# Kernel optimization log

Hardware: AMD Instinct MI355X
Metric: run time of the kernel (lower is better)

The kernel has to match this reference:

```python
import jax, jax.numpy as jnp
import numpy as np

N = 50000      # areaNum
E = 64         # embeddingsize
NE = 800000    # nonzeros of normalized adjacency
WK = 9         # walk_length + 1
L = 2          # args.L
TMP = 0.5      # args.choosing_tmp
BIAS = 1e-4


def _logistic_noise(k, shape):
    # eps ~ U(bias, 1-bias); noise = log(eps) - log(1-eps)
    u = jax.random.uniform(k, shape, minval=BIAS, maxval=1.0 - BIAS)
    return jnp.log(u) - jnp.log1p(-u)


def setup_inputs() -> dict:
    key = jax.random.key(0)
    ks = jax.random.split(key, 16)
    rng = np.random.default_rng(0)

    # ---- normalized sparse adjacency (D^-1/2 A D^-1/2), COO sorted by row ----
    row = np.sort(rng.integers(0, N, NE))
    col = rng.integers(0, N, NE)
    deg = np.bincount(row, minlength=N).astype(np.float32)
    dinv = np.where(deg > 0, deg ** -0.5, 0.0).astype(np.float32)
    vals = dinv[row] * dinv[col]

    # ---- random-walk mean-pooling adjacency, row-normalized ----
    rw_row = np.repeat(np.arange(N), WK)
    rw_col = rng.integers(0, N, N * WK)
    rw_col[::WK] = np.arange(N)  # walk starts at self
    rw_vals = np.full(N * WK, 1.0 / WK, dtype=np.float32)

    def lin(k, fan_in, shape):
        return jax.random.normal(k, shape, dtype=jnp.float32) / np.sqrt(fan_in)

    inp = {
        'x': jax.random.normal(ks[0], (N, E), dtype=jnp.float32),
        'vals': jnp.asarray(vals),
        'rw_vals': jnp.asarray(rw_vals),
        't_W1': lin(ks[1], 2 * E, (L, 2 * E, E)),
        't_b1': jnp.zeros((L, E), jnp.float32),
        't_W2': lin(ks[2], E, (L, E, 1)),
        't_b2': jnp.zeros((L, 1), jnp.float32),
        's_W1': lin(ks[3], E, (L, E, E)),
        's_b1': jnp.zeros((L, E), jnp.float32),
        's_W2': lin(ks[4], E, (L, E, 1)),
        's_b2': jnp.zeros((L, 1), jnp.float32),
        't_noise': _logistic_noise(ks[5], (L, NE)),
        's_noise': _logistic_noise(ks[6], (L, N, 1)),
        'row': jnp.asarray(row, dtype=jnp.int64) if jax.config.jax_enable_x64 else jnp.asarray(row, dtype=jnp.int32),
        'col': jnp.asarray(col, dtype=jnp.int32),
        'rw_row': jnp.asarray(rw_row, dtype=jnp.int32),
        'rw_col': jnp.asarray(rw_col, dtype=jnp.int32),
    }
    inp['row'] = jnp.asarray(row, dtype=jnp.int32)
    return inp


def reference(x, vals, rw_vals, t_W1, t_b1, t_W2, t_b2, s_W1, s_b1, s_W2, s_b2,
              t_noise, s_noise, row, col, rw_row, rw_col):
    n = x.shape[0]

    def spmm(r, c, v, h):  # sparse [n,n] @ dense [n,E]
        return jax.ops.segment_sum(v[:, None] * h[c], r, num_segments=n)

    # per-edge concat of ORIGINAL embeddings (same tensor every layer, as in source)
    t_cat = jnp.concatenate([x[row], x[col]], axis=-1)  # [nE, 2E]

    # --- mask-learning pass ---
    cur = x
    t_masks, s_masks = [], []
    for i in range(L):
        cur = spmm(row, col, vals, cur)
        t_h = jax.nn.relu(t_cat @ t_W1[i] + t_b1[i])
        t_logit = t_h @ t_W2[i] + t_b2[i]                      # [nE,1]
        t_m = jax.nn.sigmoid((t_noise[i][:, None] + t_logit) / TMP)[:, 0]
        t_masks.append(t_m)
        s_h = jax.nn.relu(cur @ s_W1[i] + s_b1[i])
        s_logit = s_h @ s_W2[i] + s_b2[i]                      # [N,1]
        s_masks.append(jax.nn.sigmoid((s_noise[i] + s_logit) / TMP))

    # --- t branch: gated spmm propagation, mean over layers ---
    cur_t = x
    acc_t = x
    for i in range(L):
        cur_t = spmm(row, col, vals * t_masks[i], cur_t)
        acc_t = acc_t + cur_t
    emb_t = acc_t / (L + 1)

    # --- s branch: gated mix with random-walk mean pooling, then spmm ---
    cur_s = x
    acc_s = x
    s_reg = jnp.float32(0.0)
    for i in range(L):
        mp = spmm(rw_row, rw_col, rw_vals, cur_s)
        cur_s = s_masks[i] * cur_s + (1.0 - s_masks[i]) * mp
        cur_s = spmm(row, col, vals, cur_s)
        acc_s = acc_s + cur_s
        s_reg = s_reg + s_masks[i].sum() / n
    emb_s = acc_s / (L + 1)
    s_reg = s_reg / L
    t_reg = jnp.float32(0.0)  # source never accumulates into t_reg
    return emb_t, emb_s, t_reg, s_reg, t_masks[-1]
```

## Files before the change

### kernel.cpp

```cpp
#include <hip/hip_runtime.h>

#define NNODES 50000
#define EDIM 64
#define WKLEN 9
#define NEDGE 800000
#define NPAD (NNODES + 64)

using bf16x8 = __attribute__((ext_vector_type(8))) __bf16;
using f32x4  = __attribute__((ext_vector_type(4))) float;

__device__ __align__(256) unsigned short g_xbf[NPAD * EDIM];
__device__ __align__(256) unsigned short g_ABh[NNODES * 128];
__device__ __align__(256) unsigned short g_c1h[NPAD * EDIM];
__device__ __align__(256) unsigned short g_c2h[NPAD * EDIM];
__device__ __align__(256) unsigned short g_g0h[NNODES * EDIM];
__device__ __align__(256) unsigned short g_sc1h[NNODES * EDIM];
__device__ __align__(256) unsigned short g_Pr[NNODES * 128];
__device__ __align__(256) unsigned short g_Pc[NNODES * 128];
__device__ __align__(256) float g_mt0[NEDGE];
__device__ __align__(256) float g_mt1[NEDGE];
__device__ __align__(256) float g_sm0[NNODES];
__device__ __align__(256) float g_sm1[NNODES];
__device__ __align__(256) int   g_rowptr[NNODES + 1];
__device__ __align__(256) unsigned short g_Tswz[2048 * 8];
__device__ __align__(256) unsigned short g_Sswz[1024 * 8];

__device__ __forceinline__ unsigned short f2bf(float f) {
    union { float f; unsigned int i; } v;
    v.f = f;
    unsigned int r = v.i + 0x7FFFu + ((v.i >> 16) & 1u);
    return (unsigned short)(r >> 16);
}
__device__ __forceinline__ float bf2f_lo(unsigned int u) {
    union { unsigned int i; float f; } v; v.i = u << 16; return v.f;
}
__device__ __forceinline__ float bf2f_hi(unsigned int u) {
    union { unsigned int i; float f; } v; v.i = u & 0xFFFF0000u; return v.f;
}

__global__ __launch_bounds__(256) void misc_kernel(
    const float* __restrict__ x, const float* __restrict__ tW1,
    const float* __restrict__ sW1, const int* __restrict__ row,
    int n, int nE)
{
    int bid = blockIdx.x, tid = threadIdx.x;
    if (bid < 1563) {
        int i = bid * 256 + tid;
        if (i < NNODES * EDIM / 8) {
            const float* src = x + i * 8;
            union { unsigned short s[8]; uint4 q; } u;
#pragma unroll
            for (int j = 0; j < 8; ++j) u.s[j] = f2bf(src[j]);
            *(uint4*)&g_xbf[i * 8] = u.q;
        }
    } else if (bid < 1759) {
        int i = (bid - 1563) * 256 + tid;
        if (i > n) return;
        int lo = 0, hi = nE;
        while (lo < hi) {
            int mid = (lo + hi) >> 1;
            if (row[mid] < i) lo = mid + 1; else hi = mid;
        }
        g_rowptr[i] = lo;
    } else if (bid < 1767) {
        int t = (bid - 1759) * 256 + tid;
        int s = t >> 9, f = (t >> 6) & 7, ln = t & 63;
        int li = s >> 1, half = s & 1, ks = f >> 2, nn = f & 3;
        int q = ln >> 4, mcl = ln & 15;
        union { unsigned short sv[8]; uint4 q4; } u;
#pragma unroll
        for (int j = 0; j < 8; ++j) {
            int kg = half * 64 + ks * 32 + q * 8 + j;
            u.sv[j] = f2bf(tW1[li * 8192 + kg * 64 + nn * 16 + mcl]);
        }
        *(uint4*)&g_Tswz[t * 8] = u.q4;
    } else {
        int t = (bid - 1767) * 256 + tid;
        int li = t >> 9, ks = (t >> 8) & 1, nn = (t >> 6) & 3, ln = t & 63;
        int q = ln >> 4, mcl = ln & 15;
        union { unsigned short sv[8]; uint4 q4; } u;
#pragma unroll
        for (int j = 0; j < 8; ++j)
            u.sv[j] = f2bf(sW1[li * 4096 + (ks * 32 + q * 8 + j) * 64 + nn * 16 + mcl]);
        *(uint4*)&g_Sswz[t * 8] = u.q4;
    }
}

__global__ __launch_bounds__(256) void prep2_kernel(int n)
{
    int tid = threadIdx.x;
    int wave = tid >> 6, lane = tid & 63;
    int mc = lane & 15, quad = lane >> 4;
    int nb = blockIdx.x * 64 + wave * 16;
    const unsigned short* bp = g_xbf + (nb + mc) * 64 + quad * 8;
    bf16x8 af0 = *(const bf16x8*)bp;
    bf16x8 af1 = *(const bf16x8*)(bp + 32);
    const f32x4 zero = {0.f, 0.f, 0.f, 0.f};
#pragma unroll
    for (int s = 0; s < 4; ++s) {
        int li = s >> 1, half = s & 1;
        f32x4 acc[4];
#pragma unroll
        for (int nn = 0; nn < 4; ++nn) acc[nn] = zero;
#pragma unroll
        for (int nn = 0; nn < 4; ++nn) {
            bf16x8 b0 = *(const bf16x8*)&g_Tswz[((s * 8 + nn) * 64 + lane) * 8];
            bf16x8 b1 = *(const bf16x8*)&g_Tswz[((s * 8 + 4 + nn) * 64 + lane) * 8];
            acc[nn] = __builtin_amdgcn_mfma_f32_16x16x32_bf16(af0, b0, acc[nn], 0, 0, 0);
            acc[nn] = __builtin_amdgcn_mfma_f32_16x16x32_bf16(af1, b1, acc[nn], 0, 0, 0);
        }
        unsigned short* dst = half ? g_Pc : g_Pr;
#pragma unroll
        for (int nn = 0; nn < 4; ++nn)
#pragma unroll
            for (int r = 0; r < 4; ++r) {
                int node = nb + quad * 4 + r;
                if (node < n)
                    dst[node * 128 + li * 64 + nn * 16 + mc] = f2bf(acc[nn][r]);
            }
    }
}

__global__ __launch_bounds__(256) void edge_mask_kernel(
    const float* __restrict__ tb1, const float* __restrict__ tW2,
    const float* __restrict__ tb2, const float* __restrict__ tnoise,
    const int* __restrict__ row, const int* __restrict__ col,
    float* __restrict__ mask_out, int nE)
{
    int tid = threadIdx.x;
    int lane = tid & 63;
    int sub = lane & 7;
    int eg = lane >> 3;
    int wv = (blockIdx.x * 256 + tid) >> 6;
    int e = wv * 8 + eg;

    float b1_0[8], b1_1[8], w2_0[8], w2_1[8];
    *(float4*)&b1_0[0] = *(const float4*)&tb1[sub * 8];
    *(float4*)&b1_0[4] = *(const float4*)&tb1[sub * 8 + 4];
    *(float4*)&b1_1[0] = *(const float4*)&tb1[64 + sub * 8];
    *(float4*)&b1_1[4] = *(const float4*)&tb1[64 + sub * 8 + 4];
    *(float4*)&w2_0[0] = *(const float4*)&tW2[sub * 8];
    *(float4*)&w2_0[4] = *(const float4*)&tW2[sub * 8 + 4];
    *(float4*)&w2_1[0] = *(const float4*)&tW2[64 + sub * 8];
    *(float4*)&w2_1[4] = *(const float4*)&tW2[64 + sub * 8 + 4];

    int rn = row[e], cn = col[e];
    uint4 qr0 = *(const uint4*)&g_Pr[rn * 128 + sub * 8];
    uint4 qr1 = *(const uint4*)&g_Pr[rn * 128 + 64 + sub * 8];
    uint4 qc0 = *(const uint4*)&g_Pc[cn * 128 + sub * 8];
    uint4 qc1 = *(const uint4*)&g_Pc[cn * 128 + 64 + sub * 8];

    float p0 = 0.f, p1 = 0.f;
    unsigned r0[4] = {qr0.x, qr0.y, qr0.z, qr0.w};
    unsigned r1[4] = {qr1.x, qr1.y, qr1.z, qr1.w};
    unsigned c0[4] = {qc0.x, qc0.y, qc0.z, qc0.w};
    unsigned c1[4] = {qc1.x, qc1.y, qc1.z, qc1.w};
#pragma unroll
    for (int k = 0; k < 4; ++k) {
        float hA = fmaxf(bf2f_lo(r0[k]) + bf2f_lo(c0[k]) + b1_0[2 * k], 0.f);
        float hB = fmaxf(bf2f_hi(r0[k]) + bf2f_hi(c0[k]) + b1_0[2 * k + 1], 0.f);
        p0 = fmaf(hA, w2_0[2 * k], p0);
        p0 = fmaf(hB, w2_0[2 * k + 1], p0);
        float gA = fmaxf(bf2f_lo(r1[k]) + bf2f_lo(c1[k]) + b1_1[2 * k], 0.f);
        float gB = fmaxf(bf2f_hi(r1[k]) + bf2f_hi(c1[k]) + b1_1[2 * k + 1], 0.f);
        p1 = fmaf(gA, w2_1[2 * k], p1);
        p1 = fmaf(gB, w2_1[2 * k + 1], p1);
    }
#pragma unroll
    for (int off = 1; off <= 4; off <<= 1) {
        p0 += __shfl_xor(p0, off, 64);
        p1 += __shfl_xor(p1, off, 64);
    }
    if (sub == 0) {
        float z0 = (tnoise[e] + p0 + tb2[0]) * 2.0f;
        float m0 = 1.0f / (1.0f + expf(-z0));
        g_mt0[e] = m0;
        float z1 = (tnoise[nE + e] + p1 + tb2[1]) * 2.0f;
        float m1 = 1.0f / (1.0f + expf(-z1));
        g_mt1[e] = m1;
        mask_out[e] = m1;
    }
}

__device__ __forceinline__ void nm_body(
    int bid, const unsigned short* __restrict__ cur, int li,
    const float* __restrict__ b1, const float* __restrict__ W2,
    const float* __restrict__ b2, const float* __restrict__ noise,
    float* __restrict__ smout, int n)
{
    int tid = threadIdx.x;
    int wave = tid >> 6, lane = tid & 63;
    int mc = lane & 15, quad = lane >> 4;
    int nb = bid * 64 + wave * 16;
    const unsigned short* basep = cur + (nb + mc) * 64 + quad * 8;
    bf16x8 af0 = *(const bf16x8*)basep;
    bf16x8 af1 = *(const bf16x8*)(basep + 32);
    f32x4 acc[4];
    const f32x4 zero = {0.f, 0.f, 0.f, 0.f};
#pragma unroll
    for (int nn = 0; nn < 4; ++nn) acc[nn] = zero;
#pragma unroll
    for (int nn = 0; nn < 4; ++nn) {
        bf16x8 b0 = *(const bf16x8*)&g_Sswz[((li * 8 + nn) * 64 + lane) * 8];
        bf16x8 b1f = *(const bf16x8*)&g_Sswz[((li * 8 + 4 + nn) * 64 + lane) * 8];
        acc[nn] = __builtin_amdgcn_mfma_f32_16x16x32_bf16(af0, b0, acc[nn], 0, 0, 0);
        acc[nn] = __builtin_amdgcn_mfma_f32_16x16x32_bf16(af1, b1f, acc[nn], 0, 0, 0);
    }
    float p[4];
#pragma unroll
    for (int r = 0; r < 4; ++r) {
        float s = 0.f;
#pragma unroll
        for (int nn = 0; nn < 4; ++nn) {
            float h = acc[nn][r] + b1[nn * 16 + mc];
            s = fmaf(fmaxf(h, 0.f), W2[nn * 16 + mc], s);
        }
        p[r] = s;
    }
#pragma unroll
    for (int off = 8; off >= 1; off >>= 1)
#pragma unroll
        for (int r = 0; r < 4; ++r) p[r] += __shfl_xor(p[r], off, 64);
    if (mc == 0) {
        float b2v = b2[0];
#pragma unroll
        for (int r = 0; r < 4; ++r) {
            int node = nb + quad * 4 + r;
            if (node < n) {
                float z = (noise[node] + p[r] + b2v) * 2.0f;
                smout[node] = 1.0f / (1.0f + expf(-z));
            }
        }
    }
}

__global__ __launch_bounds__(256) void s1_kernel(
    const int* __restrict__ colv, const float* __restrict__ vals, int n)
{
    int w = blockIdx.x * 8 + (threadIdx.x >> 5);
    int d2 = threadIdx.x & 31;
    int s = g_rowptr[w], e = g_rowptr[w + 1];
    float pl[4] = {0.f, 0.f, 0.f, 0.f}, ph[4] = {0.f, 0.f, 0.f, 0.f};
    float ql[4] = {0.f, 0.f, 0.f, 0.f}, qh[4] = {0.f, 0.f, 0.f, 0.f};
    int j = s;
    for (; j + 3 < e; j += 4) {
        int c0 = colv[j], c1 = colv[j + 1], c2 = colv[j + 2], c3 = colv[j + 3];
        unsigned u0 = *(const unsigned*)&g_xbf[c0 * 64 + 2 * d2];
        unsigned u1 = *(const unsigned*)&g_xbf[c1 * 64 + 2 * d2];
        unsigned u2 = *(const unsigned*)&g_xbf[c2 * 64 + 2 * d2];
        unsigned u3 = *(const unsigned*)&g_xbf[c3 * 64 + 2 * d2];
        float v0 = vals[j], v1 = vals[j + 1], v2 = vals[j + 2], v3 = vals[j + 3];
        float m0 = g_mt0[j], m1 = g_mt0[j + 1], m2 = g_mt0[j + 2], m3 = g_mt0[j + 3];
        float vm0 = v0 * m0, vm1 = v1 * m1, vm2 = v2 * m2, vm3 = v3 * m3;
        pl[0] = fmaf(v0, bf2f_lo(u0), pl[0]); ph[0] = fmaf(v0, bf2f_hi(u0), ph[0]);
        ql[0] = fmaf(vm0, bf2f_lo(u0), ql[0]); qh[0] = fmaf(vm0, bf2f_hi(u0), qh[0]);
        pl[1] = fmaf(v1, bf2f_lo(u1), pl[1]); ph[1] = fmaf(v1, bf2f_hi(u1), ph[1]);
        ql[1] = fmaf(vm1, bf2f_lo(u1), ql[1]); qh[1] = fmaf(vm1, bf2f_hi(u1), qh[1]);
        pl[2] = fmaf(v2, bf2f_lo(u2), pl[2]); ph[2] = fmaf(v2, bf2f_hi(u2), ph[2]);
        ql[2] = fmaf(vm2, bf2f_lo(u2), ql[2]); qh[2] = fmaf(vm2, bf2f_hi(u2), qh[2]);
        pl[3] = fmaf(v3, bf2f_lo(u3), pl[3]); ph[3] = fmaf(v3, bf2f_hi(u3), ph[3]);
        ql[3] = fmaf(vm3, bf2f_lo(u3), ql[3]); qh[3] = fmaf(vm3, bf2f_hi(u3), qh[3]);
    }
    for (; j < e; ++j) {
        int c = colv[j]; float v = vals[j], m = g_mt0[j];
        unsigned u = *(const unsigned*)&g_xbf[c * 64 + 2 * d2];
        float vm = v * m;
        pl[0] = fmaf(v, bf2f_lo(u), pl[0]); ph[0] = fmaf(v, bf2f_hi(u), ph[0]);
        ql[0] = fmaf(vm, bf2f_lo(u), ql[0]); qh[0] = fmaf(vm, bf2f_hi(u), qh[0]);
    }
    float p0 = (pl[0] + pl[1]) + (pl[2] + pl[3]);
    float p1 = (ph[0] + ph[1]) + (ph[2] + ph[3]);
    float q0 = (ql[0] + ql[1]) + (ql[2] + ql[3]);
    float q1 = (qh[0] + qh[1]) + (qh[2] + qh[3]);
    uint2 pk;
    pk.x = (unsigned)f2bf(p0) | ((unsigned)f2bf(q0) << 16);
    pk.y = (unsigned)f2bf(p1) | ((unsigned)f2bf(q1) << 16);
    *(uint2*)&g_ABh[w * 128 + 4 * d2] = pk;
    *(unsigned*)&g_c1h[w * 64 + 2 * d2] =
        (unsigned)f2bf(p0) | ((unsigned)f2bf(p1) << 16);
}

__global__ __launch_bounds__(256) void s2_nm0_kernel(
    const int* __restrict__ colv, const float* __restrict__ vals,
    const float* __restrict__ x, float* __restrict__ emb_t,
    const float* __restrict__ sb1, const float* __restrict__ sW2,
    const float* __restrict__ sb2, const float* __restrict__ snz, int n)
{
    if (blockIdx.x >= 6250) {
        nm_body(blockIdx.x - 6250, g_c1h, 0, sb1, sW2, sb2, snz, g_sm0, n);
        return;
    }
    int w = blockIdx.x * 8 + (threadIdx.x >> 5);
    int d2 = threadIdx.x & 31;
    int s = g_rowptr[w], e = g_rowptr[w + 1];
    float cl[4] = {0.f, 0.f, 0.f, 0.f}, ch[4] = {0.f, 0.f, 0.f, 0.f};
    float tl[4] = {0.f, 0.f, 0.f, 0.f}, th[4] = {0.f, 0.f, 0.f, 0.f};
    int j = s;
    for (; j + 3 < e; j += 4) {
        int c0 = colv[j], c1 = colv[j + 1], c2 = colv[j + 2], c3 = colv[j + 3];
        uint2 U0 = *(const uint2*)&g_ABh[c0 * 128 + 4 * d2];
        uint2 U1 = *(const uint2*)&g_ABh[c1 * 128 + 4 * d2];
        uint2 U2 = *(const uint2*)&g_ABh[c2 * 128 + 4 * d2];
        uint2 U3 = *(const uint2*)&g_ABh[c3 * 128 + 4 * d2];
        float v0 = vals[j], v1 = vals[j + 1], v2 = vals[j + 2], v3 = vals[j + 3];
        float m0 = g_mt1[j], m1 = g_mt1[j + 1], m2 = g_mt1[j + 2], m3 = g_mt1[j + 3];
        float vm0 = v0 * m0, vm1 = v1 * m1, vm2 = v2 * m2, vm3 = v3 * m3;
        cl[0] = fmaf(v0, bf2f_lo(U0.x), cl[0]); tl[0] = fmaf(vm0, bf2f_hi(U0.x), tl[0]);
        ch[0] = fmaf(v0, bf2f_lo(U0.y), ch[0]); th[0] = fmaf(vm0, bf2f_hi(U0.y), th[0]);
        cl[1] = fmaf(v1, bf2f_lo(U1.x), cl[1]); tl[1] = fmaf(vm1, bf2f_hi(U1.x), tl[1]);
        ch[1] = fmaf(v1, bf2f_lo(U1.y), ch[1]); th[1] = fmaf(vm1, bf2f_hi(U1.y), th[1]);
        cl[2] = fmaf(v2, bf2f_lo(U2.x), cl[2]); tl[2] = fmaf(vm2, bf2f_hi(U2.x), tl[2]);
        ch[2] = fmaf(v2, bf2f_lo(U2.y), ch[2]); th[2] = fmaf(vm2, bf2f_hi(U2.y), th[2]);
        cl[3] = fmaf(v3, bf2f_lo(U3.x), cl[3]); tl[3] = fmaf(vm3, bf2f_hi(U3.x), tl[3]);
        ch[3] = fmaf(v3, bf2f_lo(U3.y), ch[3]); th[3] = fmaf(vm3, bf2f_hi(U3.y), th[3]);
    }
    for (; j < e; ++j) {
        int c = colv[j]; float v = vals[j], m = g_mt1[j];
        uint2 U = *(const uint2*)&g_ABh[c * 128 + 4 * d2];
        float vm = v * m;
        cl[0] = fmaf(v, bf2f_lo(U.x), cl[0]); tl[0] = fmaf(vm, bf2f_hi(U.x), tl[0]);
        ch[0] = fmaf(v, bf2f_lo(U.y), ch[0]); th[0] = fmaf(vm, bf2f_hi(U.y), th[0]);
    }
    float c0s = (cl[0] + cl[1]) + (cl[2] + cl[3]);
    float c1s = (ch[0] + ch[1]) + (ch[2] + ch[3]);
    float t0s = (tl[0] + tl[1]) + (tl[2] + tl[3]);
    float t1s = (th[0] + th[1]) + (th[2] + th[3]);
    int o2 = w * 64 + 2 * d2;
    uint2 U2v = *(const uint2*)&g_ABh[w * 128 + 4 * d2];
    float2 et;
    et.x = (x[o2]     + bf2f_hi(U2v.x) + t0s) * (1.0f / 3.0f);
    et.y = (x[o2 + 1] + bf2f_hi(U2v.y) + t1s) * (1.0f / 3.0f);
    *(float2*)&emb_t[o2] = et;
    *(unsigned*)&g_c2h[o2] = (unsigned)f2bf(c0s) | ((unsigned)f2bf(c1s) << 16);
}

__device__ __forceinline__ void rw_body(
    int bid, const int* __restrict__ rw_col, const float* __restrict__ rwv,
    const unsigned short* __restrict__ cur, const float* __restrict__ smask,
    unsigned short* __restrict__ outg)
{
    int w = bid * 8 + (threadIdx.x >> 5);
    int d2 = threadIdx.x & 31;
    int base = w * WKLEN;
    float a0 = 0.f, a1 = 0.f;
#pragma unroll
    for (int j = 0; j < WKLEN; ++j) {
        int c = rw_col[base + j];
        float v = rwv[base + j];
        unsigned u = *(const unsigned*)&cur[c * 64 + 2 * d2];
        a0 = fmaf(v, bf2f_lo(u), a0);
        a1 = fmaf(v, bf2f_hi(u), a1);
    }
    float sm = smask[w];
    unsigned u = *(const unsigned*)&cur[w * 64 + 2 * d2];
    float r0 = sm * bf2f_lo(u) + (1.f - sm) * a0;
    float r1 = sm * bf2f_hi(u) + (1.f - sm) * a1;
    *(unsigned*)&outg[w * 64 + 2 * d2] =
        (unsigned)f2bf(r0) | ((unsigned)f2bf(r1) << 16);
}

__global__ __launch_bounds__(256) void rw0_nm1_kernel(
    const int* __restrict__ rw_col, const float* __restrict__ rwv,
    const float* __restrict__ sb1, const float* __restrict__ sW2,
    const float* __restrict__ sb2, const float* __restrict__ snz, int n)
{
    if (blockIdx.x >= 6250) {
        nm_body(blockIdx.x - 6250, g_c2h, 1, sb1, sW2, sb2, snz, g_sm1, n);
        return;
    }
    rw_body(blockIdx.x, rw_col, rwv, g_xbf, g_sm0, g_g0h);
}

__device__ __forceinline__ void spmm_body(
    int bid, const int* __restrict__ colv, const float* __restrict__ vals,
    const unsigned short* __restrict__ h, float* __restrict__ l0,
    float* __restrict__ l1, int* __restrict__ wout, int* __restrict__ d2out)
{
    int w = bid * 8 + (threadIdx.x >> 5);
    int d2 = threadIdx.x & 31;
    int s = g_rowptr[w], e = g_rowptr[w + 1];
    float al[4] = {0.f, 0.f, 0.f, 0.f}, ah[4] = {0.f, 0.f, 0.f, 0.f};
    int j = s;
    for (; j + 3 < e; j += 4) {
        int c0 = colv[j], c1 = colv[j + 1], c2 = colv[j + 2], c3 = colv[j + 3];
        unsigned u0 = *(const unsigned*)&h[c0 * 64 + 2 * d2];
        unsigned u1 = *(const unsigned*)&h[c1 * 64 + 2 * d2];
        unsigned u2 = *(const unsigned*)&h[c2 * 64 + 2 * d2];
        unsigned u3 = *(const unsigned*)&h[c3 * 64 + 2 * d2];
        float v0 = vals[j], v1 = vals[j + 1], v2 = vals[j + 2], v3 = vals[j + 3];
        al[0] = fmaf(v0, bf2f_lo(u0), al[0]); ah[0] = fmaf(v0, bf2f_hi(u0), ah[0]);
        al[1] = fmaf(v1, bf2f_lo(u1), al[1]); ah[1] = fmaf(v1, bf2f_hi(u1), ah[1]);
        al[2] = fmaf(v2, bf2f_lo(u2), al[2]); ah[2] = fmaf(v2, bf2f_hi(u2), ah[2]);
        al[3] = fmaf(v3, bf2f_lo(u3), al[3]); ah[3] = fmaf(v3, bf2f_hi(u3), ah[3]);
    }
    for (; j < e; ++j) {
        int c = colv[j]; float v = vals[j];
        unsigned u = *(const unsigned*)&h[c * 64 + 2 * d2];
        al[0] = fmaf(v, bf2f_lo(u), al[0]); ah[0] = fmaf(v, bf2f_hi(u), ah[0]);
    }
    *l0 = (al[0] + al[1]) + (al[2] + al[3]);
    *l1 = (ah[0] + ah[1]) + (ah[2] + ah[3]);
    *wout = w; *d2out = d2;
}

__global__ __launch_bounds__(256) void spmm10_kernel(
    const int* __restrict__ colv, const float* __restrict__ vals, int n)
{
    float a0, a1; int w, d2;
    spmm_body(blockIdx.x, colv, vals, g_g0h, &a0, &a1, &w, &d2);
    *(unsigned*)&g_sc1h[w * 64 + 2 * d2] =
        (unsigned)f2bf(a0) | ((unsigned)f2bf(a1) << 16);
}

__global__ __launch_bounds__(256) void rw1_kernel(
    const int* __restrict__ rw_col, const float* __restrict__ rwv)
{
    rw_body(blockIdx.x, rw_col, rwv, g_sc1h, g_sm1, g_g0h);
}

__global__ __launch_bounds__(256) void spmm12_fin_kernel(
    const int* __restrict__ colv, const float* __restrict__ vals,
    const float* __restrict__ x, float* __restrict__ emb_s,
    float* __restrict__ out, int n)
{
    if (blockIdx.x >= 6250) {
        __shared__ float red[256];
        float s = 0.f;
        for (int i = threadIdx.x; i < n; i += 256) s += g_sm0[i] + g_sm1[i];
        red[threadIdx.x] = s;
        __syncthreads();
        for (int off = 128; off >= 1; off >>= 1) {
            if (threadIdx.x < off) red[threadIdx.x] += red[threadIdx.x + off];
            __syncthreads();
        }
        if (threadIdx.x == 0) {
            out[6400000] = 0.0f;
            out[6400001] = red[0] / (2.0f * n);
        }
        return;
    }
    float a0, a1; int w, d2;
    spmm_body(blockIdx.x, colv, vals, g_g0h, &a0, &a1, &w, &d2);
    int o2 = w * 64 + 2 * d2;
    unsigned uc = *(const unsigned*)&g_sc1h[o2];
    float2 es;
    es.x = (x[o2]     + bf2f_lo(uc) + a0) * (1.0f / 3.0f);
    es.y = (x[o2 + 1] + bf2f_hi(uc) + a1) * (1.0f / 3.0f);
    *(float2*)&emb_s[o2] = es;
}

extern "C" void kernel_launch(void* const* d_in, const int* in_sizes, int n_in,
                              void* d_out, int out_size, void* d_ws, size_t ws_size,
                              hipStream_t stream)
{
    const float* x    = (const float*)d_in[0];
    const float* vals = (const float*)d_in[1];
    const float* rwv  = (const float*)d_in[2];
    const float* tW1  = (const float*)d_in[3];
    const float* tb1  = (const float*)d_in[4];
    const float* tW2  = (const float*)d_in[5];
    const float* tb2  = (const float*)d_in[6];
    const float* sW1  = (const float*)d_in[7];
    const float* sb1  = (const float*)d_in[8];
    const float* sW2  = (const float*)d_in[9];
    const float* sb2  = (const float*)d_in[10];
    const float* tnz  = (const float*)d_in[11];
    const float* snz  = (const float*)d_in[12];
    const int* row   = (const int*)d_in[13];
    const int* colv  = (const int*)d_in[14];
    const int* rwcol = (const int*)d_in[16];

    const int n = NNODES;
    const int nE = in_sizes[1];

    float* out   = (float*)d_out;
    float* emb_t = out;
    float* emb_s = out + 3200000;
    float* masko = out + 6400002;

    misc_kernel<<<1771, 256, 0, stream>>>(x, tW1, sW1, row, n, nE);
    prep2_kernel<<<782, 256, 0, stream>>>(n);
    edge_mask_kernel<<<nE / 32, 256, 0, stream>>>(tb1, tW2, tb2, tnz,
                                                  row, colv, masko, nE);
    s1_kernel<<<6250, 256, 0, stream>>>(colv, vals, n);
    s2_nm0_kernel<<<6250 + 782, 256, 0, stream>>>(colv, vals, x, emb_t,
                                                  sb1, sW2, sb2, snz, n);
    rw0_nm1_kernel<<<6250 + 782, 256, 0, stream>>>(rwcol, rwv,
                                                   sb1 + 64, sW2 + 64, sb2 + 1,
                                                   snz + n, n);
    spmm10_kernel<<<6250, 256, 0, stream>>>(colv, vals, n);
    rw1_kernel<<<6250, 256, 0, stream>>>(rwcol, rwv);
    spmm12_fin_kernel<<<6251, 256, 0, stream>>>(colv, vals, x, emb_s, out, n);
}
```

Measured before the change: 352.9 us.

## Cooperatively load CSR edges per row and reshuffle kernel fusion schedule

The CSR SpMM loops in s1, s2 and the shared spmm body now have each 32-lane row group load up to 32 column/value entries with one coalesced access per lane. The entries are broadcast with wave shuffles, and 8–16 gathers are issued at once for more memory-level parallelism. Kernel pairing is also reordered: nm0 runs standalone, s2 is fused with rw0, and spmm10 is fused with nm1, so dependencies still hold with the same launch count. The cost is shuffle overhead and a single accumulator chain per output in place of four, plus wasted lanes on short rows.

```diff
diff --git a/kernel.cpp b/kernel.cpp
--- a/kernel.cpp
+++ b/kernel.cpp
@@ -234,44 +234,58 @@
     }
 }
 
+__global__ __launch_bounds__(256) void nm0_kernel(
+    const float* __restrict__ sb1, const float* __restrict__ sW2,
+    const float* __restrict__ sb2, const float* __restrict__ snz, int n)
+{
+    nm_body(blockIdx.x, g_c1h, 0, sb1, sW2, sb2, snz, g_sm0, n);
+}
+
+__device__ __forceinline__ void s1_process16(
+    int sb, int d2, int myc, float myv, float myvm,
+    float& p0, float& p1, float& q0, float& q1)
+{
+    int cc[16]; float vv[16], mm[16]; unsigned uu[16];
+#pragma unroll
+    for (int k = 0; k < 16; ++k) {
+        cc[k] = __shfl(myc, sb + k, 64);
+        vv[k] = __shfl(myv, sb + k, 64);
+        mm[k] = __shfl(myvm, sb + k, 64);
+    }
+#pragma unroll
+    for (int k = 0; k < 16; ++k)
+        uu[k] = *(const unsigned*)&g_xbf[cc[k] * 64 + 2 * d2];
+#pragma unroll
+    for (int k = 0; k < 16; ++k) {
+        p0 = fmaf(vv[k], bf2f_lo(uu[k]), p0);
+        p1 = fmaf(vv[k], bf2f_hi(uu[k]), p1);
+        q0 = fmaf(mm[k], bf2f_lo(uu[k]), q0);
+        q1 = fmaf(mm[k], bf2f_hi(uu[k]), q1);
+    }
+}
+
 __global__ __launch_bounds__(256) void s1_kernel(
     const int* __restrict__ colv, const float* __restrict__ vals, int n)
 {
-    int w = blockIdx.x * 8 + (threadIdx.x >> 5);
+    int half = threadIdx.x >> 5;
+    int w = blockIdx.x * 8 + half;
+    int el = half & 1;
     int d2 = threadIdx.x & 31;
+    int sb0 = el << 5;
     int s = g_rowptr[w], e = g_rowptr[w + 1];
-    float pl[4] = {0.f, 0.f, 0.f, 0.f}, ph[4] = {0.f, 0.f, 0.f, 0.f};
-    float ql[4] = {0.f, 0.f, 0.f, 0.f}, qh[4] = {0.f, 0.f, 0.f, 0.f};
-    int j = s;
-    for (; j + 3 < e; j += 4) {
-        int c0 = colv[j], c1 = colv[j + 1], c2 = colv[j + 2], c3 = colv[j + 3];
-        unsigned u0 = *(const unsigned*)&g_xbf[c0 * 64 + 2 * d2];
-        unsigned u1 = *(const unsigned*)&g_xbf[c1 * 64 + 2 * d2];
-        unsigned u2 = *(const unsigned*)&g_xbf[c2 * 64 + 2 * d2];
-        unsigned u3 = *(const unsigned*)&g_xbf[c3 * 64 + 2 * d2];
-        float v0 = vals[j], v1 = vals[j + 1], v2 = vals[j + 2], v3 = vals[j + 3];
-        float m0 = g_mt0[j], m1 = g_mt0[j + 1], m2 = g_mt0[j + 2], m3 = g_mt0[j + 3];
-        float vm0 = v0 * m0, vm1 = v1 * m1, vm2 = v2 * m2, vm3 = v3 * m3;
-        pl[0] = fmaf(v0, bf2f_lo(u0), pl[0]); ph[0] = fmaf(v0, bf2f_hi(u0), ph[0]);
-        ql[0] = fmaf(vm0, bf2f_lo(u0), ql[0]); qh[0] = fmaf(vm0, bf2f_hi(u0), qh[0]);
-        pl[1] = fmaf(v1, bf2f_lo(u1), pl[1]); ph[1] = fmaf(v1, bf2f_hi(u1), ph[1]);
-        ql[1] = fmaf(vm1, bf2f_lo(u1), ql[1]); qh[1] = fmaf(vm1, bf2f_hi(u1), qh[1]);
-        pl[2] = fmaf(v2, bf2f_lo(u2), pl[2]); ph[2] = fmaf(v2, bf2f_hi(u2), ph[2]);
-        ql[2] = fmaf(vm2, bf2f_lo(u2), ql[2]); qh[2] = fmaf(vm2, bf2f_hi(u2), qh[2]);
-        pl[3] = fmaf(v3, bf2f_lo(u3), pl[3]); ph[3] = fmaf(v3, bf2f_hi(u3), ph[3]);
-        ql[3] = fmaf(vm3, bf2f_lo(u3), ql[3]); qh[3] = fmaf(vm3, bf2f_hi(u3), qh[3]);
-    }
-    for (; j < e; ++j) {
-        int c = colv[j]; float v = vals[j], m = g_mt0[j];
-        unsigned u = *(const unsigned*)&g_xbf[c * 64 + 2 * d2];
-        float vm = v * m;
-        pl[0] = fmaf(v, bf2f_lo(u), pl[0]); ph[0] = fmaf(v, bf2f_hi(u), ph[0]);
-        ql[0] = fmaf(vm, bf2f_lo(u), ql[0]); qh[0] = fmaf(vm, bf2f_hi(u), qh[0]);
-    }
-    float p0 = (pl[0] + pl[1]) + (pl[2] + pl[3]);
-    float p1 = (ph[0] + ph[1]) + (ph[2] + ph[3]);
-    float q0 = (ql[0] + ql[1]) + (ql[2] + ql[3]);
-    float q1 = (qh[0] + qh[1]) + (qh[2] + qh[3]);
+    float p0 = 0.f, p1 = 0.f, q0 = 0.f, q1 = 0.f;
+    for (int base = s; base < e; base += 32) {
+        int rem = e - base;
+        int myc = 0; float myv = 0.f, myvm = 0.f;
+        if (d2 < rem) {
+            myc = colv[base + d2];
+            myv = vals[base + d2];
+            myvm = myv * g_mt0[base + d2];
+        }
+        s1_process16(sb0, d2, myc, myv, myvm, p0, p1, q0, q1);
+        if (rem > 16)
+            s1_process16(sb0 + 16, d2, myc, myv, myvm, p0, p1, q0, q1);
+    }
     uint2 pk;
     pk.x = (unsigned)f2bf(p0) | ((unsigned)f2bf(q0) << 16);
     pk.y = (unsigned)f2bf(p1) | ((unsigned)f2bf(q1) << 16);
@@ -280,58 +294,27 @@
         (unsigned)f2bf(p0) | ((unsigned)f2bf(p1) << 16);
 }
 
-__global__ __launch_bounds__(256) void s2_nm0_kernel(
-    const int* __restrict__ colv, const float* __restrict__ vals,
-    const float* __restrict__ x, float* __restrict__ emb_t,
-    const float* __restrict__ sb1, const float* __restrict__ sW2,
-    const float* __restrict__ sb2, const float* __restrict__ snz, int n)
-{
-    if (blockIdx.x >= 6250) {
-        nm_body(blockIdx.x - 6250, g_c1h, 0, sb1, sW2, sb2, snz, g_sm0, n);
-        return;
-    }
-    int w = blockIdx.x * 8 + (threadIdx.x >> 5);
-    int d2 = threadIdx.x & 31;
-    int s = g_rowptr[w], e = g_rowptr[w + 1];
-    float cl[4] = {0.f, 0.f, 0.f, 0.f}, ch[4] = {0.f, 0.f, 0.f, 0.f};
-    float tl[4] = {0.f, 0.f, 0.f, 0.f}, th[4] = {0.f, 0.f, 0.f, 0.f};
-    int j = s;
-    for (; j + 3 < e; j += 4) {
-        int c0 = colv[j], c1 = colv[j + 1], c2 = colv[j + 2], c3 = colv[j + 3];
-        uint2 U0 = *(const uint2*)&g_ABh[c0 * 128 + 4 * d2];
-        uint2 U1 = *(const uint2*)&g_ABh[c1 * 128 + 4 * d2];
-        uint2 U2 = *(const uint2*)&g_ABh[c2 * 128 + 4 * d2];
-        uint2 U3 = *(const uint2*)&g_ABh[c3 * 128 + 4 * d2];
-        float v0 = vals[j], v1 = vals[j + 1], v2 = vals[j + 2], v3 = vals[j + 3];
-        float m0 = g_mt1[j], m1 = g_mt1[j + 1], m2 = g_mt1[j + 2], m3 = g_mt1[j + 3];
-        float vm0 = v0 * m0, vm1 = v1 * m1, vm2 = v2 * m2, vm3 = v3 * m3;
-        cl[0] = fmaf(v0, bf2f_lo(U0.x), cl[0]); tl[0] = fmaf(vm0, bf2f_hi(U0.x), tl[0]);
-        ch[0] = fmaf(v0, bf2f_lo(U0.y), ch[0]); th[0] = fmaf(vm0, bf2f_hi(U0.y), th[0]);
-        cl[1] = fmaf(v1, bf2f_lo(U1.x), cl[1]); tl[1] = fmaf(vm1, bf2f_hi(U1.x), tl[1]);
-        ch[1] = fmaf(v1, bf2f_lo(U1.y), ch[1]); th[1] = fmaf(vm1, bf2f_hi(U1.y), th[1]);
-        cl[2] = fmaf(v2, bf2f_lo(U2.x), cl[2]); tl[2] = fmaf(vm2, bf2f_hi(U2.x), tl[2]);
-        ch[2] = fmaf(v2, bf2f_lo(U2.y), ch[2]); th[2] = fmaf(vm2, bf2f_hi(U2.y), th[2]);
-        cl[3] = fmaf(v3, bf2f_lo(U3.x), cl[3]); tl[3] = fmaf(vm3, bf2f_hi(U3.x), tl[3]);
-        ch[3] = fmaf(v3, bf2f_lo(U3.y), ch[3]); th[3] = fmaf(vm3, bf2f_hi(U3.y), th[3]);
-    }
-    for (; j < e; ++j) {
-        int c = colv[j]; float v = vals[j], m = g_mt1[j];
-        uint2 U = *(const uint2*)&g_ABh[c * 128 + 4 * d2];
-        float vm = v * m;
-        cl[0] = fmaf(v, bf2f_lo(U.x), cl[0]); tl[0] = fmaf(vm, bf2f_hi(U.x), tl[0]);
-        ch[0] = fmaf(v, bf2f_lo(U.y), ch[0]); th[0] = fmaf(vm, bf2f_hi(U.y), th[0]);
-    }
-    float c0s = (cl[0] + cl[1]) + (cl[2] + cl[3]);
-    float c1s = (ch[0] + ch[1]) + (ch[2] + ch[3]);
-    float t0s = (tl[0] + tl[1]) + (tl[2] + tl[3]);
-    float t1s = (th[0] + th[1]) + (th[2] + th[3]);
-    int o2 = w * 64 + 2 * d2;
-    uint2 U2v = *(const uint2*)&g_ABh[w * 128 + 4 * d2];
-    float2 et;
-    et.x = (x[o2]     + bf2f_hi(U2v.x) + t0s) * (1.0f / 3.0f);
-    et.y = (x[o2 + 1] + bf2f_hi(U2v.y) + t1s) * (1.0f / 3.0f);
-    *(float2*)&emb_t[o2] = et;
-    *(unsigned*)&g_c2h[o2] = (unsigned)f2bf(c0s) | ((unsigned)f2bf(c1s) << 16);
+__device__ __forceinline__ void s2_process8(
+    int sb, int d2, int myc, float myv, float myvm,
+    float& c0, float& c1, float& t0, float& t1)
+{
+    int cc[8]; float vv[8], mm[8]; uint2 uu[8];
+#pragma unroll
+    for (int k = 0; k < 8; ++k) {
+        cc[k] = __shfl(myc, sb + k, 64);
+        vv[k] = __shfl(myv, sb + k, 64);
+        mm[k] = __shfl(myvm, sb + k, 64);
+    }
+#pragma unroll
+    for (int k = 0; k < 8; ++k)
+        uu[k] = *(const uint2*)&g_ABh[cc[k] * 128 + 4 * d2];
+#pragma unroll
+    for (int k = 0; k < 8; ++k) {
+        c0 = fmaf(vv[k], bf2f_lo(uu[k].x), c0);
+        t0 = fmaf(mm[k], bf2f_hi(uu[k].x), t0);
+        c1 = fmaf(vv[k], bf2f_lo(uu[k].y), c1);
+        t1 = fmaf(mm[k], bf2f_hi(uu[k].y), t1);
+    }
 }
 
 __device__ __forceinline__ void rw_body(
@@ -359,16 +342,62 @@
         (unsigned)f2bf(r0) | ((unsigned)f2bf(r1) << 16);
 }
 
-__global__ __launch_bounds__(256) void rw0_nm1_kernel(
+__global__ __launch_bounds__(256) void s2_rw0_kernel(
+    const int* __restrict__ colv, const float* __restrict__ vals,
     const int* __restrict__ rw_col, const float* __restrict__ rwv,
-    const float* __restrict__ sb1, const float* __restrict__ sW2,
-    const float* __restrict__ sb2, const float* __restrict__ snz, int n)
+    const float* __restrict__ x, float* __restrict__ emb_t, int n)
 {
     if (blockIdx.x >= 6250) {
-        nm_body(blockIdx.x - 6250, g_c2h, 1, sb1, sW2, sb2, snz, g_sm1, n);
+        rw_body(blockIdx.x - 6250, rw_col, rwv, g_xbf, g_sm0, g_g0h);
         return;
     }
-    rw_body(blockIdx.x, rw_col, rwv, g_xbf, g_sm0, g_g0h);
+    int half = threadIdx.x >> 5;
+    int w = blockIdx.x * 8 + half;
+    int el = half & 1;
+    int d2 = threadIdx.x & 31;
+    int sb0 = el << 5;
+    int s = g_rowptr[w], e = g_rowptr[w + 1];
+    float c0 = 0.f, c1 = 0.f, t0 = 0.f, t1 = 0.f;
+    for (int base = s; base < e; base += 32) {
+        int rem = e - base;
+        int myc = 0; float myv = 0.f, myvm = 0.f;
+        if (d2 < rem) {
+            myc = colv[base + d2];
+            myv = vals[base + d2];
+            myvm = myv * g_mt1[base + d2];
+        }
+        s2_process8(sb0, d2, myc, myv, myvm, c0, c1, t0, t1);
+        if (rem > 8)  s2_process8(sb0 + 8,  d2, myc, myv, myvm, c0, c1, t0, t1);
+        if (rem > 16) s2_process8(sb0 + 16, d2, myc, myv, myvm, c0, c1, t0, t1);
+        if (rem > 24) s2_process8(sb0 + 24, d2, myc, myv, myvm, c0, c1, t0, t1);
+    }
+    int o2 = w * 64 + 2 * d2;
+    uint2 U2v = *(const uint2*)&g_ABh[w * 128 + 4 * d2];
+    float2 et;
+    et.x = (x[o2]     + bf2f_hi(U2v.x) + t0) * (1.0f / 3.0f);
+    et.y = (x[o2 + 1] + bf2f_hi(U2v.y) + t1) * (1.0f / 3.0f);
+    *(float2*)&emb_t[o2] = et;
+    *(unsigned*)&g_c2h[o2] = (unsigned)f2bf(c0) | ((unsigned)f2bf(c1) << 16);
+}
+
+__device__ __forceinline__ void sp_process16(
+    const unsigned short* __restrict__ h, int sb, int d2,
+    int myc, float myv, float& a0, float& a1)
+{
+    int cc[16]; float vv[16]; unsigned uu[16];
+#pragma unroll
+    for (int k = 0; k < 16; ++k) {
+        cc[k] = __shfl(myc, sb + k, 64);
+        vv[k] = __shfl(myv, sb + k, 64);
+    }
+#pragma unroll
+    for (int k = 0; k < 16; ++k)
+        uu[k] = *(const unsigned*)&h[cc[k] * 64 + 2 * d2];
+#pragma unroll
+    for (int k = 0; k < 16; ++k) {
+        a0 = fmaf(vv[k], bf2f_lo(uu[k]), a0);
+        a1 = fmaf(vv[k], bf2f_hi(uu[k]), a1);
+    }
 }
 
 __device__ __forceinline__ void spmm_body(
@@ -376,36 +405,35 @@
     const unsigned short* __restrict__ h, float* __restrict__ l0,
     float* __restrict__ l1, int* __restrict__ wout, int* __restrict__ d2out)
 {
-    int w = bid * 8 + (threadIdx.x >> 5);
+    int half = threadIdx.x >> 5;
+    int w = bid * 8 + half;
+    int el = half & 1;
     int d2 = threadIdx.x & 31;
+    int sb0 = el << 5;
     int s = g_rowptr[w], e = g_rowptr[w + 1];
-    float al[4] = {0.f, 0.f, 0.f, 0.f}, ah[4] = {0.f, 0.f, 0.f, 0.f};
-    int j = s;
-    for (; j + 3 < e; j += 4) {
-        int c0 = colv[j], c1 = colv[j + 1], c2 = colv[j + 2], c3 = colv[j + 3];
-        unsigned u0 = *(const unsigned*)&h[c0 * 64 + 2 * d2];
-        unsigned u1 = *(const unsigned*)&h[c1 * 64 + 2 * d2];
-        unsigned u2 = *(const unsigned*)&h[c2 * 64 + 2 * d2];
-        unsigned u3 = *(const unsigned*)&h[c3 * 64 + 2 * d2];
-        float v0 = vals[j], v1 = vals[j + 1], v2 = vals[j + 2], v3 = vals[j + 3];
-        al[0] = fmaf(v0, bf2f_lo(u0), al[0]); ah[0] = fmaf(v0, bf2f_hi(u0), ah[0]);
-        al[1] = fmaf(v1, bf2f_lo(u1), al[1]); ah[1] = fmaf(v1, bf2f_hi(u1), ah[1]);
-        al[2] = fmaf(v2, bf2f_lo(u2), al[2]); ah[2] = fmaf(v2, bf2f_hi(u2), ah[2]);
-        al[3] = fmaf(v3, bf2f_lo(u3), al[3]); ah[3] = fmaf(v3, bf2f_hi(u3), ah[3]);
-    }
-    for (; j < e; ++j) {
-        int c = colv[j]; float v = vals[j];
-        unsigned u = *(const unsigned*)&h[c * 64 + 2 * d2];
-        al[0] = fmaf(v, bf2f_lo(u), al[0]); ah[0] = fmaf(v, bf2f_hi(u), ah[0]);
-    }
-    *l0 = (al[0] + al[1]) + (al[2] + al[3]);
-    *l1 = (ah[0] + ah[1]) + (ah[2] + ah[3]);
-    *wout = w; *d2out = d2;
-}
-
-__global__ __launch_bounds__(256) void spmm10_kernel(
-    const int* __restrict__ colv, const float* __restrict__ vals, int n)
-{
+    float a0 = 0.f, a1 = 0.f;
+    for (int base = s; base < e; base += 32) {
+        int rem = e - base;
+        int myc = 0; float myv = 0.f;
+        if (d2 < rem) {
+            myc = colv[base + d2];
+            myv = vals[base + d2];
+        }
+        sp_process16(h, sb0, d2, myc, myv, a0, a1);
+        if (rem > 16) sp_process16(h, sb0 + 16, d2, myc, myv, a0, a1);
+    }
+    *l0 = a0; *l1 = a1; *wout = w; *d2out = d2;
+}
+
+__global__ __launch_bounds__(256) void spmm10_nm1_kernel(
+    const int* __restrict__ colv, const float* __restrict__ vals,
+    const float* __restrict__ sb1, const float* __restrict__ sW2,
+    const float* __restrict__ sb2, const float* __restrict__ snz, int n)
+{
+    if (blockIdx.x >= 6250) {
+        nm_body(blockIdx.x - 6250, g_c2h, 1, sb1, sW2, sb2, snz, g_sm1, n);
+        return;
+    }
     float a0, a1; int w, d2;
     spmm_body(blockIdx.x, colv, vals, g_g0h, &a0, &a1, &w, &d2);
     *(unsigned*)&g_sc1h[w * 64 + 2 * d2] =
@@ -483,12 +511,11 @@
     edge_mask_kernel<<<nE / 32, 256, 0, stream>>>(tb1, tW2, tb2, tnz,
                                                   row, colv, masko, nE);
     s1_kernel<<<6250, 256, 0, stream>>>(colv, vals, n);
-    s2_nm0_kernel<<<6250 + 782, 256, 0, stream>>>(colv, vals, x, emb_t,
-                                                  sb1, sW2, sb2, snz, n);
-    rw0_nm1_kernel<<<6250 + 782, 256, 0, stream>>>(rwcol, rwv,
-                                                   sb1 + 64, sW2 + 64, sb2 + 1,
-                                                   snz + n, n);
-    spmm10_kernel<<<6250, 256, 0, stream>>>(colv, vals, n);
+    nm0_kernel<<<782, 256, 0, stream>>>(sb1, sW2, sb2, snz, n);
+    s2_rw0_kernel<<<12500, 256, 0, stream>>>(colv, vals, rwcol, rwv, x, emb_t, n);
+    spmm10_nm1_kernel<<<6250 + 782, 256, 0, stream>>>(colv, vals,
+                                                      sb1 + 64, sW2 + 64, sb2 + 1,
+                                                      snz + n, n);
     rw1_kernel<<<6250, 256, 0, stream>>>(rwcol, rwv);
     spmm12_fin_kernel<<<6251, 256, 0, stream>>>(colv, vals, x, emb_s, out, n);
 }
```

Result: faster. 343.7 us (-2.6%).
